# Kernel optimization log

Measured on AMD Instinct MI355X. Metric: run time of the kernel, lower is better.

## Reference

```python
import jax, jax.numpy as jnp
import numpy as np

B, IN, H1, H2, OUT, P = 8192, 1024, 2048, 2048, 1024, 8


def setup_inputs() -> dict:
    key = jax.random.key(0)
    ks = jax.random.split(key, 12)
    s = 0.02
    return {
        "x": jax.random.normal(ks[0], (B, IN), dtype=jnp.float32),
        # layer 1: P expert linears (stacked) + selector
        "W1": jax.random.normal(ks[1], (P, IN, H1), dtype=jnp.float32) * s,
        "b1": jax.random.normal(ks[2], (P, H1), dtype=jnp.float32) * s,
        "S1": jax.random.normal(ks[3], (IN, P), dtype=jnp.float32) * s,
        "sb1": jax.random.normal(ks[4], (P,), dtype=jnp.float32) * s,
        # layer 2
        "W2": jax.random.normal(ks[5], (P, H1, H2), dtype=jnp.float32) * s,
        "b2": jax.random.normal(ks[6], (P, H2), dtype=jnp.float32) * s,
        "S2": jax.random.normal(ks[7], (H1, P), dtype=jnp.float32) * s,
        "sb2": jax.random.normal(ks[8], (P,), dtype=jnp.float32) * s,
        # classifier
        "Wc": jax.random.normal(ks[9], (H2, OUT), dtype=jnp.float32) * s,
        "bc": jax.random.normal(ks[10], (OUT,), dtype=jnp.float32) * s,
    }


def _drn_layer(x, W, b, S, sb):
    # selector + softmax routing probs: [B, P]
    probs = jax.nn.softmax(x @ S + sb, axis=-1)
    # all-expert dense outputs: [B, P, O]
    outs = jnp.einsum('bi,pio->bpo', x, W) + b[None, :, :]
    # soft-weighted combine over experts
    return jnp.einsum('bpo,bp->bo', outs, probs)


def reference(x, W1, b1, S1, sb1, W2, b2, S2, sb2, Wc, bc):
    h = jax.nn.relu(_drn_layer(x, W1, b1, S1, sb1))
    h = jax.nn.relu(_drn_layer(h, W2, b2, S2, sb2))
    return h @ Wc + bc
```

## Files before the change

kernel.cpp:

```cpp
#include <hip/hip_runtime.h>
#include <hip/hip_bf16.h>

#define B_SZ   8192
#define IN_SZ  1024
#define H1_SZ  2048
#define H2_SZ  2048
#define OUT_SZ 1024
#define NP     8

typedef __bf16 bf16x8 __attribute__((ext_vector_type(8)));
typedef float  f32x4  __attribute__((ext_vector_type(4)));

__device__ __forceinline__ void async_ld16(const void* g, void* l) {
    __builtin_amdgcn_global_load_lds(
        (const __attribute__((address_space(1))) unsigned int*)g,
        (__attribute__((address_space(3))) unsigned int*)l,
        16, 0, 0);
}

__device__ __forceinline__ float bfbits_to_f(unsigned int u) {
    union { unsigned int i; float f; } c;
    c.i = u << 16;
    return c.f;
}

__global__ void transpose_cast_k(const float* __restrict__ in, __hip_bfloat16* __restrict__ out,
                                 int K, int N) {
    __shared__ float tile[32][33];
    int n0 = blockIdx.x * 32, k0 = blockIdx.y * 32;
    int tx = threadIdx.x, ty = threadIdx.y;
#pragma unroll
    for (int j = 0; j < 4; ++j)
        tile[ty + j * 8][tx] = in[(size_t)(k0 + ty + j * 8) * N + (n0 + tx)];
    __syncthreads();
#pragma unroll
    for (int j = 0; j < 4; ++j) {
        int nn = ty + j * 8;
        out[(size_t)(n0 + nn) * K + (k0 + tx)] = __float2bfloat16(tile[tx][nn]);
    }
}

template <typename T>
__global__ void selector_k(const T* __restrict__ in, const float* __restrict__ S,
                           const float* __restrict__ sb, float* __restrict__ probs, int K) {
    int row  = blockIdx.x * blockDim.y + threadIdx.y;
    int lane = threadIdx.x;
    float acc[NP];
#pragma unroll
    for (int p = 0; p < NP; ++p) acc[p] = 0.f;
    const T* xr = in + (size_t)row * K;
    for (int k = lane; k < K; k += 64) {
        float xv;
        if constexpr (sizeof(T) == 2) xv = __bfloat162float(xr[k]);
        else                          xv = (float)xr[k];
        const float* sr = S + (size_t)k * NP;
#pragma unroll
        for (int p = 0; p < NP; ++p) acc[p] += xv * sr[p];
    }
#pragma unroll
    for (int p = 0; p < NP; ++p)
#pragma unroll
        for (int off = 32; off > 0; off >>= 1)
            acc[p] += __shfl_down(acc[p], off, 64);
    if (lane == 0) {
        float v[NP], m = -1e30f;
#pragma unroll
        for (int p = 0; p < NP; ++p) { v[p] = acc[p] + sb[p]; m = fmaxf(m, v[p]); }
        float s = 0.f;
#pragma unroll
        for (int p = 0; p < NP; ++p) { v[p] = expf(v[p] - m); s += v[p]; }
        float inv = 1.f / s;
#pragma unroll
        for (int p = 0; p < NP; ++p) probs[(size_t)row * NP + p] = v[p] * inv;
    }
}

template <typename T>
__global__ void build_a_k(const T* __restrict__ in, const float* __restrict__ probs,
                          __hip_bfloat16* __restrict__ A, int K) {
    int b = blockIdx.y;
    int i = (blockIdx.x * 128 + threadIdx.x) * 8;
    float pv[NP];
#pragma unroll
    for (int p = 0; p < NP; ++p) pv[p] = probs[(size_t)b * NP + p];
    float xv[8];
    if constexpr (sizeof(T) == 2) {
        uint4 u = *(const uint4*)((const unsigned short*)in + (size_t)b * K + i);
        xv[0] = bfbits_to_f(u.x & 0xffff); xv[1] = bfbits_to_f(u.x >> 16);
        xv[2] = bfbits_to_f(u.y & 0xffff); xv[3] = bfbits_to_f(u.y >> 16);
        xv[4] = bfbits_to_f(u.z & 0xffff); xv[5] = bfbits_to_f(u.z >> 16);
        xv[6] = bfbits_to_f(u.w & 0xffff); xv[7] = bfbits_to_f(u.w >> 16);
    } else {
        const float* xp = (const float*)in + (size_t)b * K + i;
        float4 f0 = *(const float4*)xp;
        float4 f1 = *(const float4*)(xp + 4);
        xv[0] = f0.x; xv[1] = f0.y; xv[2] = f0.z; xv[3] = f0.w;
        xv[4] = f1.x; xv[5] = f1.y; xv[6] = f1.z; xv[7] = f1.w;
    }
    size_t base = (size_t)b * ((size_t)NP * K);
#pragma unroll
    for (int p = 0; p < NP; ++p) {
        __hip_bfloat16 tmp[8];
#pragma unroll
        for (int j = 0; j < 8; ++j) tmp[j] = __float2bfloat16(pv[p] * xv[j]);
        uint4 u4;
        __builtin_memcpy(&u4, tmp, 16);
        *(uint4*)(A + base + (size_t)p * K + i) = u4;
    }
}

__global__ __launch_bounds__(512, 2)
void drn_gemm8_k(const __hip_bfloat16* __restrict__ A, const __hip_bfloat16* __restrict__ Wt,
                 int N, int K, const float* __restrict__ probs,
                 const float* __restrict__ bexp, __hip_bfloat16* __restrict__ C) {
    __shared__ alignas(16) char smem[131072];

    const int tid  = threadIdx.x;
    const int wid  = tid >> 6, lane = tid & 63;
    const int quad = lane >> 4, l16 = lane & 15;
    const int wr = wid >> 2, wc = wid & 3;

    const int g   = blockIdx.x;
    const int cpx = gridDim.x >> 3;
    const int wg  = (g & 7) * cpx + (g >> 3);
    const int nbn = N >> 8;
    const int mb  = wg / nbn, nb = wg % nbn;
    const int m0  = mb * 256, n0 = nb * 256;

    const int arow = tid >> 3;
    const int gsw  = ((tid & 7) ^ (arow & 7)) << 3;
    const __hip_bfloat16* Ag = A  + (size_t)(m0 + arow) * K + gsw;
    const __hip_bfloat16* Bg = Wt + (size_t)(n0 + arow) * K + gsw;
    const size_t r64 = (size_t)64 * K;
    char* aDst = smem + wid * 1024;
    char* bDst = smem + 65536 + wid * 1024;

#define STG_A(dbuf, ksrc, h) do {                                              \
    const __hip_bfloat16* s_ = Ag + (size_t)(ksrc) * 64 + (size_t)(2*(h)) * r64; \
    char* d_ = aDst + (dbuf) * 32768 + (h) * 16384;                            \
    async_ld16(s_,       d_);                                                  \
    async_ld16(s_ + r64, d_ + 8192); } while (0)
#define STG_B(dbuf, ksrc, h) do {                                              \
    const __hip_bfloat16* s_ = Bg + (size_t)(ksrc) * 64 + (size_t)(2*(h)) * r64; \
    char* d_ = bDst + (dbuf) * 32768 + (h) * 16384;                            \
    async_ld16(s_,       d_);                                                  \
    async_ld16(s_ + r64, d_ + 8192); } while (0)

    const int csw  = (quad ^ (l16 & 7)) << 4;
    const int aoff = (wr * 128 + l16) * 128 + csw;
    const int boff = 65536 + (wc * 64 + l16) * 128 + csw;

#define LDA(dst, dbuf, m, k) dst = *(const bf16x8*)(smem + (dbuf) * 32768 + ((aoff ^ ((k) << 6)) + (m) * 2048))
#define LDB(dst, dbuf, n, k) dst = *(const bf16x8*)(smem + (dbuf) * 32768 + ((boff ^ ((k) << 6)) + (n) * 2048))

#define LD_A2(dbuf, mq)                               \
    LDA(af[0][0], dbuf, 2*(mq),     0); LDA(af[0][1], dbuf, 2*(mq),     1); \
    LDA(af[1][0], dbuf, 2*(mq) + 1, 0); LDA(af[1][1], dbuf, 2*(mq) + 1, 1)
#define LD_B8(dbuf)                                   \
    LDB(bfr[0][0], dbuf, 0, 0); LDB(bfr[0][1], dbuf, 0, 1); \
    LDB(bfr[1][0], dbuf, 1, 0); LDB(bfr[1][1], dbuf, 1, 1); \
    LDB(bfr[2][0], dbuf, 2, 0); LDB(bfr[2][1], dbuf, 2, 1); \
    LDB(bfr[3][0], dbuf, 3, 0); LDB(bfr[3][1], dbuf, 3, 1)

#define PH_SYNC()                                          \
    __builtin_amdgcn_s_barrier();                          \
    asm volatile("s_waitcnt lgkmcnt(0)" ::: "memory");     \
    __builtin_amdgcn_sched_barrier(0)

#define PH_MFMA(q) do {                                    \
    __builtin_amdgcn_s_setprio(1);                         \
    _Pragma("unroll")                                      \
    for (int ml = 0; ml < 2; ++ml)                         \
      _Pragma("unroll")                                    \
      for (int n_ = 0; n_ < 4; ++n_)                       \
        _Pragma("unroll")                                  \
        for (int k_ = 0; k_ < 2; ++k_)                     \
          acc[2*(q)+ml][n_] = __builtin_amdgcn_mfma_f32_16x16x32_bf16( \
              af[ml][k_], bfr[n_][k_], acc[2*(q)+ml][n_], 0, 0, 0);    \
    __builtin_amdgcn_s_setprio(0); } while (0)

#define PH_END()                                           \
    __builtin_amdgcn_s_barrier();                          \
    __builtin_amdgcn_sched_barrier(0)

#define PH_END_VM()                                        \
    asm volatile("s_waitcnt vmcnt(4)" ::: "memory");       \
    __builtin_amdgcn_s_barrier();                          \
    __builtin_amdgcn_sched_barrier(0)

    f32x4 zero = {0.f, 0.f, 0.f, 0.f};
    f32x4 acc[8][4];
#pragma unroll
    for (int m = 0; m < 8; ++m)
#pragma unroll
        for (int n = 0; n < 4; ++n) acc[m][n] = zero;

    const int NT = K >> 6;
    const int NI = NT >> 1;

    STG_A(0, 0, 0); STG_A(0, 0, 1);
    STG_B(0, 0, 0); STG_B(0, 0, 1);
    STG_B(1, 1, 0); STG_B(1, 1, 1);
    asm volatile("s_waitcnt vmcnt(4)" ::: "memory");
    __builtin_amdgcn_s_barrier();
    __builtin_amdgcn_sched_barrier(0);

    bf16x8 af[2][2], bfr[4][2];

    for (int i = 0; i < NI; ++i) {
        const int T  = 2 * i;
        const int k2 = (T + 2 < NT) ? T + 2 : NT - 1;
        const int k3 = (T + 3 < NT) ? T + 3 : NT - 1;

        LD_B8(0); LD_A2(0, 0);
        STG_A(1, T + 1, 0);
        PH_SYNC(); PH_MFMA(0); PH_END();

        LD_A2(0, 1);
        STG_A(1, T + 1, 1);
        PH_SYNC(); PH_MFMA(1); PH_END();

        LD_A2(0, 2);
        STG_B(0, k2, 0);
        PH_SYNC(); PH_MFMA(2); PH_END();

        LD_A2(0, 3);
        STG_B(0, k2, 1);
        PH_SYNC(); PH_MFMA(3); PH_END_VM();

        LD_B8(1); LD_A2(1, 0);
        STG_A(0, k2, 0);
        PH_SYNC(); PH_MFMA(0); PH_END();

        LD_A2(1, 1);
        STG_A(0, k2, 1);
        PH_SYNC(); PH_MFMA(1); PH_END();

        LD_A2(1, 2);
        STG_B(1, k3, 0);
        PH_SYNC(); PH_MFMA(2); PH_END();

        LD_A2(1, 3);
        STG_B(1, k3, 1);
        PH_SYNC(); PH_MFMA(3); PH_END_VM();
    }

    asm volatile("s_waitcnt vmcnt(0)" ::: "memory");

    const int colb = n0 + wc * 64 + l16;
    float bx[4][NP];
#pragma unroll
    for (int n = 0; n < 4; ++n)
#pragma unroll
        for (int p = 0; p < NP; ++p)
            bx[n][p] = bexp[(size_t)p * N + colb + n * 16];
#pragma unroll
    for (int m = 0; m < 8; ++m) {
#pragma unroll
        for (int r = 0; r < 4; ++r) {
            const int row = m0 + wr * 128 + m * 16 + quad * 4 + r;
            const float* pr = probs + (size_t)row * NP;
            f32x4 p0 = *(const f32x4*)pr;
            f32x4 p1 = *(const f32x4*)(pr + 4);
            float pv[NP] = {p0[0], p0[1], p0[2], p0[3], p1[0], p1[1], p1[2], p1[3]};
#pragma unroll
            for (int n = 0; n < 4; ++n) {
                float bsum = 0.f;
#pragma unroll
                for (int p = 0; p < NP; ++p) bsum += pv[p] * bx[n][p];
                float v = fmaxf(acc[m][n][r] + bsum, 0.f);
                C[(size_t)row * N + colb + n * 16] = __float2bfloat16(v);
            }
        }
    }
#undef STG_A
#undef STG_B
#undef LDA
#undef LDB
#undef LD_A2
#undef LD_B8
#undef PH_SYNC
#undef PH_MFMA
#undef PH_END
#undef PH_END_VM
}

__global__ __launch_bounds__(256)
void gemm_bt_k(const __hip_bfloat16* __restrict__ A, const __hip_bfloat16* __restrict__ Bt,
               int M, int N, int K, const float* __restrict__ bias, float* __restrict__ C) {
    __shared__ alignas(16) __hip_bfloat16 As[2 * 128 * 32];
    __shared__ alignas(16) __hip_bfloat16 Bs[2 * 128 * 32];
    const int tid  = threadIdx.x;
    const int wid  = tid >> 6, lane = tid & 63;
    const int quad = lane >> 4, l16 = lane & 15;
    const int waveM = (wid >> 1) << 6, waveN = (wid & 1) << 6;
    const int m0 = blockIdx.x * 128, n0 = blockIdx.y * 128;

    f32x4 zero = {0.f, 0.f, 0.f, 0.f};
    f32x4 acc[4][4];
#pragma unroll
    for (int a = 0; a < 4; ++a)
#pragma unroll
        for (int b = 0; b < 4; ++b) acc[a][b] = zero;

    const int srow = tid >> 2;
    const int skc  = (((tid & 3) ^ (srow & 3) ^ ((srow >> 2) & 3)) << 3);
    const __hip_bfloat16* Ag = A  + (size_t)(m0 + srow) * K + skc;
    const __hip_bfloat16* Bg = Bt + (size_t)(n0 + srow) * K + skc;
    const size_t rowStep = (size_t)64 * K;
    __hip_bfloat16* AsB = As + wid * 512;
    __hip_bfloat16* BsB = Bs + wid * 512;
    const int csel = (quad ^ (l16 & 3) ^ ((l16 >> 2) & 3)) << 3;

    async_ld16(Ag,           AsB);
    async_ld16(Ag + rowStep, AsB + 2048);
    async_ld16(Bg,           BsB);
    async_ld16(Bg + rowStep, BsB + 2048);

    for (int kt = 0; kt < K; kt += 32) {
        const int cur = (kt >> 5) & 1;
        __syncthreads();
        if (kt + 32 < K) {
            const int nb = (1 - cur) * 4096;
            async_ld16(Ag + kt + 32,           AsB + nb);
            async_ld16(Ag + kt + 32 + rowStep, AsB + nb + 2048);
            async_ld16(Bg + kt + 32,           BsB + nb);
            async_ld16(Bg + kt + 32 + rowStep, BsB + nb + 2048);
        }
        const __hip_bfloat16* AsC = As + cur * 4096;
        const __hip_bfloat16* BsC = Bs + cur * 4096;
        bf16x8 af[4], bfr[4];
#pragma unroll
        for (int q = 0; q < 4; ++q) {
            af[q]  = *(const bf16x8*)(AsC + (waveM + q * 16 + l16) * 32 + csel);
            bfr[q] = *(const bf16x8*)(BsC + (waveN + q * 16 + l16) * 32 + csel);
        }
#pragma unroll
        for (int tm = 0; tm < 4; ++tm)
#pragma unroll
            for (int tn = 0; tn < 4; ++tn)
                acc[tm][tn] = __builtin_amdgcn_mfma_f32_16x16x32_bf16(
                    af[tm], bfr[tn], acc[tm][tn], 0, 0, 0);
    }

    const int colb = n0 + waveN + l16;
#pragma unroll
    for (int tm = 0; tm < 4; ++tm)
#pragma unroll
        for (int r = 0; r < 4; ++r) {
            int row = m0 + waveM + tm * 16 + quad * 4 + r;
#pragma unroll
            for (int tn = 0; tn < 4; ++tn)
                C[(size_t)row * N + colb + tn * 16] =
                    acc[tm][tn][r] + bias[colb + tn * 16];
        }
}

extern "C" void kernel_launch(void* const* d_in, const int* in_sizes, int n_in,
                              void* d_out, int out_size, void* d_ws, size_t ws_size,
                              hipStream_t stream) {
    const float* x   = (const float*)d_in[0];
    const float* W1  = (const float*)d_in[1];
    const float* b1  = (const float*)d_in[2];
    const float* S1  = (const float*)d_in[3];
    const float* sb1 = (const float*)d_in[4];
    const float* W2  = (const float*)d_in[5];
    const float* b2  = (const float*)d_in[6];
    const float* S2  = (const float*)d_in[7];
    const float* sb2 = (const float*)d_in[8];
    const float* Wc  = (const float*)d_in[9];
    const float* bc  = (const float*)d_in[10];
    float* out = (float*)d_out;

    char* ws = (char*)d_ws;
    size_t off = 0;
    auto alloc = [&](size_t bytes) {
        char* p = ws + off;
        off += (bytes + 255) & ~(size_t)255;
        return p;
    };
    __hip_bfloat16* W1t = (__hip_bfloat16*)alloc((size_t)H1_SZ * (NP * IN_SZ) * 2);
    __hip_bfloat16* W2t = (__hip_bfloat16*)alloc((size_t)H2_SZ * (NP * H1_SZ) * 2);
    __hip_bfloat16* Wct = (__hip_bfloat16*)alloc((size_t)OUT_SZ * H2_SZ * 2);
    float* probs1       = (float*)alloc((size_t)B_SZ * NP * 4);
    float* probs2       = (float*)alloc((size_t)B_SZ * NP * 4);
    __hip_bfloat16* h1  = (__hip_bfloat16*)alloc((size_t)B_SZ * H1_SZ * 2);
    __hip_bfloat16* h2  = (__hip_bfloat16*)alloc((size_t)B_SZ * H2_SZ * 2);
    __hip_bfloat16* Abuf= (__hip_bfloat16*)alloc((size_t)B_SZ * (NP * H1_SZ) * 2);

    dim3 tb(32, 8);
    transpose_cast_k<<<dim3(H1_SZ / 32, (NP * IN_SZ) / 32), tb, 0, stream>>>(W1, W1t, NP * IN_SZ, H1_SZ);
    transpose_cast_k<<<dim3(H2_SZ / 32, (NP * H1_SZ) / 32), tb, 0, stream>>>(W2, W2t, NP * H1_SZ, H2_SZ);
    transpose_cast_k<<<dim3(OUT_SZ / 32, H2_SZ / 32), tb, 0, stream>>>(Wc, Wct, H2_SZ, OUT_SZ);

    selector_k<float><<<B_SZ / 4, dim3(64, 4), 0, stream>>>(x, S1, sb1, probs1, IN_SZ);
    build_a_k<float><<<dim3(IN_SZ / 1024, B_SZ), 128, 0, stream>>>(x, probs1, Abuf, IN_SZ);
    drn_gemm8_k<<<(B_SZ / 256) * (H1_SZ / 256), 512, 0, stream>>>(
        Abuf, W1t, H1_SZ, NP * IN_SZ, probs1, b1, h1);

    selector_k<__hip_bfloat16><<<B_SZ / 4, dim3(64, 4), 0, stream>>>(h1, S2, sb2, probs2, H1_SZ);
    build_a_k<__hip_bfloat16><<<dim3(H1_SZ / 1024, B_SZ), 128, 0, stream>>>(h1, probs2, Abuf, H1_SZ);
    drn_gemm8_k<<<(B_SZ / 256) * (H2_SZ / 256), 512, 0, stream>>>(
        Abuf, W2t, H2_SZ, NP * H1_SZ, probs2, b2, h2);

    gemm_bt_k<<<dim3(B_SZ / 128, OUT_SZ / 128), 256, 0, stream>>>(
        h2, Wct, B_SZ, OUT_SZ, H2_SZ, bc, out);
}
```

Before: 1.042 ms.

## Drop prob-scaled A buffer by rescaling accumulator with expert probability ratios

Removes the build_a_k pass that materialised an [B, P*K] prob-scaled bf16 activation matrix. The GEMM now reads the unscaled activation directly, wrapping the A k-index per expert. After each expert's K-segment it multiplies the accumulator by p_e/p_{e+1}, and by p_last after the final expert, which telescopes to the weighted sum. This saves a large write and read of the A buffer per layer. It adds a cast kernel for x and vectorises the transpose stores. The risk is numerical blow-up when a ratio of probabilities is extreme.

```diff
diff --git a/kernel.cpp b/kernel.cpp
--- a/kernel.cpp
+++ b/kernel.cpp
@@ -18,10 +18,18 @@
         16, 0, 0);
 }
 
-__device__ __forceinline__ float bfbits_to_f(unsigned int u) {
-    union { unsigned int i; float f; } c;
-    c.i = u << 16;
-    return c.f;
+__global__ void cast_bf16_k(const float* __restrict__ in, __hip_bfloat16* __restrict__ out) {
+    size_t i = ((size_t)blockIdx.x * 256 + threadIdx.x) * 8;
+    float4 f0 = *(const float4*)(in + i);
+    float4 f1 = *(const float4*)(in + i + 4);
+    __hip_bfloat16 t[8] = {
+        __float2bfloat16(f0.x), __float2bfloat16(f0.y),
+        __float2bfloat16(f0.z), __float2bfloat16(f0.w),
+        __float2bfloat16(f1.x), __float2bfloat16(f1.y),
+        __float2bfloat16(f1.z), __float2bfloat16(f1.w)};
+    uint4 u4;
+    __builtin_memcpy(&u4, t, 16);
+    *(uint4*)(out + i) = u4;
 }
 
 __global__ void transpose_cast_k(const float* __restrict__ in, __hip_bfloat16* __restrict__ out,
@@ -33,16 +41,22 @@
     for (int j = 0; j < 4; ++j)
         tile[ty + j * 8][tx] = in[(size_t)(k0 + ty + j * 8) * N + (n0 + tx)];
     __syncthreads();
-#pragma unroll
-    for (int j = 0; j < 4; ++j) {
-        int nn = ty + j * 8;
-        out[(size_t)(n0 + nn) * K + (k0 + tx)] = __float2bfloat16(tile[tx][nn]);
+    const int kk = (tx & 15) * 2;
+#pragma unroll
+    for (int j = 0; j < 2; ++j) {
+        int nn = ty + j * 8 + (tx >> 4) * 16;
+        __hip_bfloat16 t2[2] = {__float2bfloat16(tile[kk][nn]),
+                                __float2bfloat16(tile[kk + 1][nn])};
+        unsigned int u;
+        __builtin_memcpy(&u, t2, 4);
+        *(unsigned int*)(out + (size_t)(n0 + nn) * K + (k0 + kk)) = u;
     }
 }
 
 template <typename T>
 __global__ void selector_k(const T* __restrict__ in, const float* __restrict__ S,
-                           const float* __restrict__ sb, float* __restrict__ probs, int K) {
+                           const float* __restrict__ sb, float* __restrict__ probs,
+                           float* __restrict__ ratT, int K) {
     int row  = blockIdx.x * blockDim.y + threadIdx.y;
     int lane = threadIdx.x;
     float acc[NP];
@@ -72,47 +86,18 @@
         float inv = 1.f / s;
 #pragma unroll
         for (int p = 0; p < NP; ++p) probs[(size_t)row * NP + p] = v[p] * inv;
-    }
-}
-
-template <typename T>
-__global__ void build_a_k(const T* __restrict__ in, const float* __restrict__ probs,
-                          __hip_bfloat16* __restrict__ A, int K) {
-    int b = blockIdx.y;
-    int i = (blockIdx.x * 128 + threadIdx.x) * 8;
-    float pv[NP];
-#pragma unroll
-    for (int p = 0; p < NP; ++p) pv[p] = probs[(size_t)b * NP + p];
-    float xv[8];
-    if constexpr (sizeof(T) == 2) {
-        uint4 u = *(const uint4*)((const unsigned short*)in + (size_t)b * K + i);
-        xv[0] = bfbits_to_f(u.x & 0xffff); xv[1] = bfbits_to_f(u.x >> 16);
-        xv[2] = bfbits_to_f(u.y & 0xffff); xv[3] = bfbits_to_f(u.y >> 16);
-        xv[4] = bfbits_to_f(u.z & 0xffff); xv[5] = bfbits_to_f(u.z >> 16);
-        xv[6] = bfbits_to_f(u.w & 0xffff); xv[7] = bfbits_to_f(u.w >> 16);
-    } else {
-        const float* xp = (const float*)in + (size_t)b * K + i;
-        float4 f0 = *(const float4*)xp;
-        float4 f1 = *(const float4*)(xp + 4);
-        xv[0] = f0.x; xv[1] = f0.y; xv[2] = f0.z; xv[3] = f0.w;
-        xv[4] = f1.x; xv[5] = f1.y; xv[6] = f1.z; xv[7] = f1.w;
-    }
-    size_t base = (size_t)b * ((size_t)NP * K);
-#pragma unroll
-    for (int p = 0; p < NP; ++p) {
-        __hip_bfloat16 tmp[8];
-#pragma unroll
-        for (int j = 0; j < 8; ++j) tmp[j] = __float2bfloat16(pv[p] * xv[j]);
-        uint4 u4;
-        __builtin_memcpy(&u4, tmp, 16);
-        *(uint4*)(A + base + (size_t)p * K + i) = u4;
-    }
-}
-
+#pragma unroll
+        for (int p = 0; p < NP - 1; ++p) ratT[(size_t)p * B_SZ + row] = v[p] / v[p + 1];
+        ratT[(size_t)(NP - 1) * B_SZ + row] = v[NP - 1] * inv;
+    }
+}
+
+template <int TPS>
 __global__ __launch_bounds__(512, 2)
 void drn_gemm8_k(const __hip_bfloat16* __restrict__ A, const __hip_bfloat16* __restrict__ Wt,
-                 int N, int K, const float* __restrict__ probs,
-                 const float* __restrict__ bexp, __hip_bfloat16* __restrict__ C) {
+                 int N, int K, int Kin, const float* __restrict__ ratT,
+                 const float* __restrict__ probs, const float* __restrict__ bexp,
+                 __hip_bfloat16* __restrict__ C) {
     __shared__ alignas(16) char smem[131072];
 
     const int tid  = threadIdx.x;
@@ -129,22 +114,23 @@
 
     const int arow = tid >> 3;
     const int gsw  = ((tid & 7) ^ (arow & 7)) << 3;
-    const __hip_bfloat16* Ag = A  + (size_t)(m0 + arow) * K + gsw;
+    const __hip_bfloat16* Ag = A  + (size_t)(m0 + arow) * Kin + gsw;
     const __hip_bfloat16* Bg = Wt + (size_t)(n0 + arow) * K + gsw;
-    const size_t r64 = (size_t)64 * K;
+    const size_t r64a = (size_t)64 * Kin;
+    const size_t r64b = (size_t)64 * K;
     char* aDst = smem + wid * 1024;
     char* bDst = smem + 65536 + wid * 1024;
 
 #define STG_A(dbuf, ksrc, h) do {                                              \
-    const __hip_bfloat16* s_ = Ag + (size_t)(ksrc) * 64 + (size_t)(2*(h)) * r64; \
+    const __hip_bfloat16* s_ = Ag + (((ksrc) & (TPS - 1)) * 64) + (size_t)(2*(h)) * r64a; \
     char* d_ = aDst + (dbuf) * 32768 + (h) * 16384;                            \
-    async_ld16(s_,       d_);                                                  \
-    async_ld16(s_ + r64, d_ + 8192); } while (0)
+    async_ld16(s_,        d_);                                                 \
+    async_ld16(s_ + r64a, d_ + 8192); } while (0)
 #define STG_B(dbuf, ksrc, h) do {                                              \
-    const __hip_bfloat16* s_ = Bg + (size_t)(ksrc) * 64 + (size_t)(2*(h)) * r64; \
+    const __hip_bfloat16* s_ = Bg + ((size_t)(ksrc) * 64) + (size_t)(2*(h)) * r64b; \
     char* d_ = bDst + (dbuf) * 32768 + (h) * 16384;                            \
-    async_ld16(s_,       d_);                                                  \
-    async_ld16(s_ + r64, d_ + 8192); } while (0)
+    async_ld16(s_,        d_);                                                 \
+    async_ld16(s_ + r64b, d_ + 8192); } while (0)
 
     const int csw  = (quad ^ (l16 & 7)) << 4;
     const int aoff = (wr * 128 + l16) * 128 + csw;
@@ -243,6 +229,19 @@
         LD_A2(1, 3);
         STG_B(1, k3, 1);
         PH_SYNC(); PH_MFMA(3); PH_END_VM();
+
+        if (((i + 1) & (TPS / 2 - 1)) == 0) {
+            const int p = (i + 1) / (TPS / 2) - 1;
+            const float* rp = ratT + (size_t)p * B_SZ + (m0 + wr * 128 + quad * 4);
+            f32x4 rr[8];
+#pragma unroll
+            for (int m = 0; m < 8; ++m) rr[m] = *(const f32x4*)(rp + m * 16);
+#pragma unroll
+            for (int m = 0; m < 8; ++m)
+#pragma unroll
+                for (int n = 0; n < 4; ++n)
+                    acc[m][n] *= rr[m];
+        }
     }
 
     asm volatile("s_waitcnt vmcnt(0)" ::: "memory");
@@ -384,24 +383,25 @@
     __hip_bfloat16* Wct = (__hip_bfloat16*)alloc((size_t)OUT_SZ * H2_SZ * 2);
     float* probs1       = (float*)alloc((size_t)B_SZ * NP * 4);
     float* probs2       = (float*)alloc((size_t)B_SZ * NP * 4);
+    float* rat1         = (float*)alloc((size_t)NP * B_SZ * 4);
+    float* rat2         = (float*)alloc((size_t)NP * B_SZ * 4);
+    __hip_bfloat16* xbf = (__hip_bfloat16*)alloc((size_t)B_SZ * IN_SZ * 2);
     __hip_bfloat16* h1  = (__hip_bfloat16*)alloc((size_t)B_SZ * H1_SZ * 2);
     __hip_bfloat16* h2  = (__hip_bfloat16*)alloc((size_t)B_SZ * H2_SZ * 2);
-    __hip_bfloat16* Abuf= (__hip_bfloat16*)alloc((size_t)B_SZ * (NP * H1_SZ) * 2);
 
     dim3 tb(32, 8);
     transpose_cast_k<<<dim3(H1_SZ / 32, (NP * IN_SZ) / 32), tb, 0, stream>>>(W1, W1t, NP * IN_SZ, H1_SZ);
     transpose_cast_k<<<dim3(H2_SZ / 32, (NP * H1_SZ) / 32), tb, 0, stream>>>(W2, W2t, NP * H1_SZ, H2_SZ);
     transpose_cast_k<<<dim3(OUT_SZ / 32, H2_SZ / 32), tb, 0, stream>>>(Wc, Wct, H2_SZ, OUT_SZ);
-
-    selector_k<float><<<B_SZ / 4, dim3(64, 4), 0, stream>>>(x, S1, sb1, probs1, IN_SZ);
-    build_a_k<float><<<dim3(IN_SZ / 1024, B_SZ), 128, 0, stream>>>(x, probs1, Abuf, IN_SZ);
-    drn_gemm8_k<<<(B_SZ / 256) * (H1_SZ / 256), 512, 0, stream>>>(
-        Abuf, W1t, H1_SZ, NP * IN_SZ, probs1, b1, h1);
-
-    selector_k<__hip_bfloat16><<<B_SZ / 4, dim3(64, 4), 0, stream>>>(h1, S2, sb2, probs2, H1_SZ);
-    build_a_k<__hip_bfloat16><<<dim3(H1_SZ / 1024, B_SZ), 128, 0, stream>>>(h1, probs2, Abuf, H1_SZ);
-    drn_gemm8_k<<<(B_SZ / 256) * (H2_SZ / 256), 512, 0, stream>>>(
-        Abuf, W2t, H2_SZ, NP * H1_SZ, probs2, b2, h2);
+    cast_bf16_k<<<(B_SZ * IN_SZ) / (256 * 8), 256, 0, stream>>>(x, xbf);
+
+    selector_k<float><<<B_SZ / 4, dim3(64, 4), 0, stream>>>(x, S1, sb1, probs1, rat1, IN_SZ);
+    drn_gemm8_k<16><<<(B_SZ / 256) * (H1_SZ / 256), 512, 0, stream>>>(
+        xbf, W1t, H1_SZ, NP * IN_SZ, IN_SZ, rat1, probs1, b1, h1);
+
+    selector_k<__hip_bfloat16><<<B_SZ / 4, dim3(64, 4), 0, stream>>>(h1, S2, sb2, probs2, rat2, H1_SZ);
+    drn_gemm8_k<32><<<(B_SZ / 256) * (H2_SZ / 256), 512, 0, stream>>>(
+        h1, W2t, H2_SZ, NP * H1_SZ, H1_SZ, rat2, probs2, b2, h2);
 
     gemm_bt_k<<<dim3(B_SZ / 128, OUT_SZ / 128), 256, 0, stream>>>(
         h2, Wct, B_SZ, OUT_SZ, H2_SZ, bc, out);
```

Result: no change. 1.036 ms (-0.6%).
